# Performance work log

Hardware: AMD Instinct MI355X
Metric: run time of the kernel (lower is better)

Reference implementation:

```python
import jax, jax.numpy as jnp
import numpy as np

N_NODES = 10000
N_EDGES = 160000
N_HEADS = 2
N_IN = 16   # fc input dim = x channels (15) + 1 dist channel
N_OUT = 32
ALPHA = 0.2
B, T_LEN = 2, 8


def setup_inputs() -> dict:
    key = jax.random.key(0)
    ks = jax.random.split(key, 6)
    x = jax.random.normal(ks[0], (B, T_LEN, N_NODES, N_IN - 1), dtype=jnp.float32)
    d_ew = jax.random.uniform(ks[1], (N_EDGES + N_NODES, N_HEADS), dtype=jnp.float32)
    u_edges = jax.random.randint(ks[2], (N_EDGES, 2), 0, N_NODES, dtype=jnp.int64)
    u_dist = jax.random.uniform(ks[3], (N_EDGES,), dtype=jnp.float32)
    W = jax.random.normal(ks[4], (N_OUT, N_IN), dtype=jnp.float32) * (1.0 / np.sqrt(N_IN))
    b = jax.random.normal(ks[5], (N_OUT,), dtype=jnp.float32) * 0.01
    return {"x": x, "T": T_LEN, "d_ew": d_ew, "u_edges": u_edges,
            "u_dist": u_dist, "W": W, "b": b}


def reference(x, T, d_ew, u_edges, u_dist, W, b):
    # d_edges = [u_edges; self-loops], d_dist = [u_dist; zeros]
    loops = jnp.arange(N_NODES, dtype=u_edges.dtype)
    d_edges = jnp.concatenate([u_edges, jnp.stack([loops, loops], axis=1)], axis=0)
    d_dist = jnp.concatenate([u_dist, jnp.zeros((N_NODES,), dtype=u_dist.dtype)], axis=0)
    node_i, node_j = d_edges[:, 0], d_edges[:, 1]

    Bx, t, _, C = x.shape
    # graph convolution: out[:, :, j] = sum_e{j(e)=j} d_ew[e] * x[:, :, i(e)]
    xg = x[:, :, node_i, :]                               # (B, t, E, C)
    msgs = xg[..., None, :] * d_ew[None, None, :, :, None]  # (B, t, E, H, C)
    x_conv = jnp.zeros((Bx, t, N_NODES, N_HEADS, C), dtype=x.dtype)
    x_conv = x_conv.at[:, :, node_j].add(msgs)            # (B, t, N, H, C)

    # dist convolution: (N, H)
    dist_conv = jnp.zeros((N_NODES, N_HEADS), dtype=d_ew.dtype)
    dist_conv = dist_conv.at[node_j].add(d_dist[:, None] * d_ew)

    # concat dist channel, broadcast over (B, t)
    dist_b = jnp.broadcast_to(dist_conv[None, None, :, :, None],
                              (Bx, t, N_NODES, N_HEADS, 1))
    x_feature = jnp.concatenate([x_conv, dist_b], axis=-1)  # (B, t, N, H, C+1)

    x_out = jnp.einsum('btnhc,oc->btnho', x_feature, W) + b

    # temporal alpha-blend (RHS uses pre-update values, as in torch slice assign)
    x_out = jnp.concatenate(
        [x_out[:, :1], ALPHA * x_out[:, :-1] + (1.0 - ALPHA) * x_out[:, 1:]], axis=1)
    return jax.nn.sigmoid(x_out)
```

## Files before the change

### kernel.cpp

```cpp
#include <hip/hip_runtime.h>
#include <hip/hip_bf16.h>

#define NN 10000
#define NE 160000
#define NBT 16
#define CIN 15
#define HPAD 128
#define BCAP 64
#define NOUT 32
#define ALPHA_F 0.2f

#define TRANS_BLKS 625
#define EDGE_BLKS  625

__device__ __forceinline__ float bf2f(unsigned short u) {
    return __uint_as_float(((unsigned int)u) << 16);
}
__device__ __forceinline__ unsigned short f2bf(float f) {
    __hip_bfloat16 h = __float2bfloat16(f);
    return *(unsigned short*)&h;
}

__global__ __launch_bounds__(256) void zero_ws(int* __restrict__ p) {
    int i = blockIdx.x * 256 + threadIdx.x;
    if (i < NN) p[i] = 0;
}

__global__ __launch_bounds__(256) void prep(const float* __restrict__ x,
                                            const int* __restrict__ edges,
                                            const float* __restrict__ dist,
                                            const float* __restrict__ dew,
                                            unsigned short* __restrict__ xh,
                                            int* __restrict__ cursor,
                                            int2* __restrict__ epay) {
    __shared__ float tile[NBT][16 * CIN];
    int bid = blockIdx.x;
    int tid = threadIdx.x;
    if (bid < TRANS_BLKS) {
        int n0 = bid * 16;
        if (tid < 16 * CIN) {
#pragma unroll
            for (int bt = 0; bt < NBT; ++bt)
                tile[bt][tid] = x[((size_t)bt * NN + n0) * CIN + tid];
        }
        __syncthreads();
        for (int g = tid; g < 16 * 256; g += 256) {
            int ln = g >> 8;
            int r  = g & 255;
            int c  = r & 15;
            int bt = r >> 4;
            float v = (c < 15) ? tile[bt][ln * CIN + c] : 0.f;
            xh[(size_t)(n0 + ln) * 256 + r] = f2bf(v);
        }
    } else {
        int e = (bid - TRANS_BLKS) * 256 + tid;
        if (e < NE) {
            int2 ed = ((const int2*)edges)[e];
            float2 w = ((const float2*)dew)[e];
            float d = dist[e];
            int pos = atomicAdd(&cursor[ed.y], 1);
            if (pos < BCAP) {
                unsigned int px = (unsigned int)ed.x | ((unsigned int)f2bf(d) << 16);
                unsigned int py = (unsigned int)f2bf(w.x) | ((unsigned int)f2bf(w.y) << 16);
                epay[ed.y * BCAP + pos] = make_int2((int)px, (int)py);
            }
        }
    }
}

__global__ __launch_bounds__(256) void fused_node(const unsigned short* __restrict__ xh,
                                                  const int* __restrict__ cursor,
                                                  const int2* __restrict__ epay,
                                                  const float* __restrict__ dew,
                                                  const float* __restrict__ W,
                                                  const float* __restrict__ bias,
                                                  float* __restrict__ out) {
    __shared__ float s_xc[4][2][256];

    const int tid = threadIdx.x;
    const int unit = tid >> 6;
    const int lane = tid & 63;
    const int n = blockIdx.x * 4 + unit;
    const int o = lane & 31;
    const int h = lane >> 5;

    float4 w0_ = *(const float4*)(W + o * 16);
    float4 w1_ = *(const float4*)(W + o * 16 + 4);
    float4 w2_ = *(const float4*)(W + o * 16 + 8);
    float4 w3_ = *(const float4*)(W + o * 16 + 12);
    float bo = bias[o];

    int deg = cursor[n];
    if (deg > BCAP) deg = BCAP;

    int2 pay = epay[n * BCAP + lane];

    float dd  = bf2f((unsigned short)((unsigned int)pay.x >> 16));
    float w0l = bf2f((unsigned short)((unsigned int)pay.y & 0xFFFFu));
    float w1l = bf2f((unsigned short)((unsigned int)pay.y >> 16));
    float dc0 = (lane < deg) ? dd * w0l : 0.f;
    float dc1 = (lane < deg) ? dd * w1l : 0.f;
#pragma unroll
    for (int m = 32; m; m >>= 1) {
        dc0 += __shfl_xor(dc0, m, 64);
        dc1 += __shfl_xor(dc1, m, 64);
    }

    const char* xbase = (const char*)xh + 8 * lane;
    float a00 = 0.f, a01 = 0.f, a02 = 0.f, a03 = 0.f;
    float a10 = 0.f, a11 = 0.f, a12 = 0.f, a13 = 0.f;
#pragma unroll 8
    for (int k = 0; k < deg; ++k) {
        int sx = __builtin_amdgcn_readlane(pay.x, k);
        int sw = __builtin_amdgcn_readlane(pay.y, k);
        uint2 u = *(const uint2*)(xbase + (size_t)((sx & 0xFFFF) << 9));
        float x0 = __uint_as_float(u.x << 16);
        float x1 = __uint_as_float(u.x & 0xFFFF0000u);
        float x2 = __uint_as_float(u.y << 16);
        float x3 = __uint_as_float(u.y & 0xFFFF0000u);
        float w0 = __uint_as_float((unsigned int)sw << 16);
        float w1 = __uint_as_float((unsigned int)sw & 0xFFFF0000u);
        a00 += w0 * x0; a01 += w0 * x1; a02 += w0 * x2; a03 += w0 * x3;
        a10 += w1 * x0; a11 += w1 * x1; a12 += w1 * x2; a13 += w1 * x3;
    }
    {
        uint2 u = *(const uint2*)(xbase + ((size_t)n << 9));
        float w0 = dew[2 * (NE + n) + 0];
        float w1 = dew[2 * (NE + n) + 1];
        float x0 = __uint_as_float(u.x << 16);
        float x1 = __uint_as_float(u.x & 0xFFFF0000u);
        float x2 = __uint_as_float(u.y << 16);
        float x3 = __uint_as_float(u.y & 0xFFFF0000u);
        a00 += w0 * x0; a01 += w0 * x1; a02 += w0 * x2; a03 += w0 * x3;
        a10 += w1 * x0; a11 += w1 * x1; a12 += w1 * x2; a13 += w1 * x3;
    }
    *(float4*)&s_xc[unit][0][4 * lane] = make_float4(a00, a01, a02, a03);
    *(float4*)&s_xc[unit][1][4 * lane] = make_float4(a10, a11, a12, a13);

    asm volatile("s_waitcnt lgkmcnt(0)" ::: "memory");

    {
        float Wr[16] = { w0_.x, w0_.y, w0_.z, w0_.w,
                         w1_.x, w1_.y, w1_.z, w1_.w,
                         w2_.x, w2_.y, w2_.z, w2_.w,
                         w3_.x, w3_.y, w3_.z, w3_.w };
        float base = bo + Wr[15] * (h ? dc1 : dc0);
        const float* xc = s_xc[unit][h];
#pragma unroll
        for (int b = 0; b < 2; ++b) {
            float prev = 0.f;
#pragma unroll
            for (int t = 0; t < 8; ++t) {
                const float* xt = xc + b * HPAD + t * 16;
                float4 v0 = *(const float4*)(xt);
                float4 v1 = *(const float4*)(xt + 4);
                float4 v2 = *(const float4*)(xt + 8);
                float4 v3 = *(const float4*)(xt + 12);
                float y = base;
                y += Wr[0]*v0.x + Wr[1]*v0.y + Wr[2]*v0.z + Wr[3]*v0.w;
                y += Wr[4]*v1.x + Wr[5]*v1.y + Wr[6]*v1.z + Wr[7]*v1.w;
                y += Wr[8]*v2.x + Wr[9]*v2.y + Wr[10]*v2.z + Wr[11]*v2.w;
                y += Wr[12]*v3.x + Wr[13]*v3.y + Wr[14]*v3.z + Wr[15]*v3.w;
                float v = (t == 0) ? y : (ALPHA_F * prev + (1.f - ALPHA_F) * y);
                float sg = 1.f / (1.f + __expf(-v));
                __builtin_nontemporal_store(sg,
                    &out[(((size_t)(b * 8 + t) * NN + n) * 2 + h) * NOUT + o]);
                prev = y;
            }
        }
    }
}

extern "C" void kernel_launch(void* const* d_in, const int* in_sizes, int n_in,
                              void* d_out, int out_size, void* d_ws, size_t ws_size,
                              hipStream_t stream) {
    const float* x     = (const float*)d_in[0];
    const float* dew   = (const float*)d_in[2];
    const int*   edges = (const int*)d_in[3];
    const float* dist  = (const float*)d_in[4];
    const float* W     = (const float*)d_in[5];
    const float* bias  = (const float*)d_in[6];
    float* out = (float*)d_out;

    unsigned short* xh = (unsigned short*)d_ws;
    int2* epay   = (int2*)(xh + (size_t)NN * 256);
    int* cursor  = (int*)(epay + (size_t)NN * BCAP);

    zero_ws<<<(NN + 255) / 256, 256, 0, stream>>>(cursor);
    prep<<<TRANS_BLKS + EDGE_BLKS, 256, 0, stream>>>(x, edges, dist, dew,
                                                     xh, cursor, epay);
    fused_node<<<2500, 256, 0, stream>>>(xh, cursor, epay, dew, W, bias, out);
}
```

Baseline: 49.99 us.

## Process two nodes per wavefront in fused node kernel to increase gather ILP

Each 64-lane wavefront now handles two destination nodes, with each half-wave loading one node's edge payload. The gather loop interleaves two independent edge streams, so more loads are in flight per iteration. Grid size is halved accordingly. In exchange it uses more registers, pays for the max of the two degrees, and adds an overflow path for degree above 32.

```diff
diff --git a/kernel.cpp b/kernel.cpp
--- a/kernel.cpp
+++ b/kernel.cpp
@@ -75,14 +75,16 @@
                                                   const float* __restrict__ W,
                                                   const float* __restrict__ bias,
                                                   float* __restrict__ out) {
-    __shared__ float s_xc[4][2][256];
-
-    const int tid = threadIdx.x;
+    __shared__ float s_xc[4][2][2][256];
+
+    const int tid  = threadIdx.x;
     const int unit = tid >> 6;
     const int lane = tid & 63;
-    const int n = blockIdx.x * 4 + unit;
-    const int o = lane & 31;
-    const int h = lane >> 5;
+    const int sub  = lane & 31;
+    const int h    = lane >> 5;
+    const int o    = lane & 31;
+    const int nA   = blockIdx.x * 8 + unit * 2;
+    const int nB   = nA + 1;
 
     float4 w0_ = *(const float4*)(W + o * 16);
     float4 w1_ = *(const float4*)(W + o * 16 + 4);
@@ -90,82 +92,171 @@
     float4 w3_ = *(const float4*)(W + o * 16 + 12);
     float bo = bias[o];
 
-    int deg = cursor[n];
-    if (deg > BCAP) deg = BCAP;
-
-    int2 pay = epay[n * BCAP + lane];
-
-    float dd  = bf2f((unsigned short)((unsigned int)pay.x >> 16));
-    float w0l = bf2f((unsigned short)((unsigned int)pay.y & 0xFFFFu));
-    float w1l = bf2f((unsigned short)((unsigned int)pay.y >> 16));
-    float dc0 = (lane < deg) ? dd * w0l : 0.f;
-    float dc1 = (lane < deg) ? dd * w1l : 0.f;
-#pragma unroll
-    for (int m = 32; m; m >>= 1) {
-        dc0 += __shfl_xor(dc0, m, 64);
-        dc1 += __shfl_xor(dc1, m, 64);
+    int degA = cursor[nA]; degA = degA > BCAP ? BCAP : degA;
+    int degB = cursor[nB]; degB = degB > BCAP ? BCAP : degB;
+    const int myN   = h ? nB : nA;
+    const int myDeg = h ? degB : degA;
+
+    int2 pay  = epay[myN * BCAP + sub];
+    int2 pay2 = make_int2(0, 0);
+    if (degA > 32 || degB > 32)
+        pay2 = epay[myN * BCAP + 32 + sub];
+
+    float dc0, dc1;
+    {
+        float dd  = bf2f((unsigned short)((unsigned int)pay.x >> 16));
+        float w0l = bf2f((unsigned short)((unsigned int)pay.y & 0xFFFFu));
+        float w1l = bf2f((unsigned short)((unsigned int)pay.y >> 16));
+        dc0 = (sub < myDeg) ? dd * w0l : 0.f;
+        dc1 = (sub < myDeg) ? dd * w1l : 0.f;
+        float dd2 = bf2f((unsigned short)((unsigned int)pay2.x >> 16));
+        float w02 = bf2f((unsigned short)((unsigned int)pay2.y & 0xFFFFu));
+        float w12 = bf2f((unsigned short)((unsigned int)pay2.y >> 16));
+        if (sub + 32 < myDeg) { dc0 += dd2 * w02; dc1 += dd2 * w12; }
+#pragma unroll
+        for (int m = 16; m; m >>= 1) {
+            dc0 += __shfl_xor(dc0, m, 64);
+            dc1 += __shfl_xor(dc1, m, 64);
+        }
     }
 
     const char* xbase = (const char*)xh + 8 * lane;
-    float a00 = 0.f, a01 = 0.f, a02 = 0.f, a03 = 0.f;
-    float a10 = 0.f, a11 = 0.f, a12 = 0.f, a13 = 0.f;
-#pragma unroll 8
-    for (int k = 0; k < deg; ++k) {
-        int sx = __builtin_amdgcn_readlane(pay.x, k);
-        int sw = __builtin_amdgcn_readlane(pay.y, k);
-        uint2 u = *(const uint2*)(xbase + (size_t)((sx & 0xFFFF) << 9));
+    float aA0=0,aA1=0,aA2=0,aA3=0,aA4=0,aA5=0,aA6=0,aA7=0;
+    float aB0=0,aB1=0,aB2=0,aB3=0,aB4=0,aB5=0,aB6=0,aB7=0;
+
+    int dmax  = degA > degB ? degA : degB;
+    int dmain = dmax > 32 ? 32 : dmax;
+#pragma unroll 4
+    for (int k = 0; k < dmain; ++k) {
+        {
+            int kk = (k < degA) ? k : 0;
+            unsigned int px = (unsigned int)__builtin_amdgcn_readlane(pay.x, kk);
+            unsigned int pw = (unsigned int)__builtin_amdgcn_readlane(pay.y, kk);
+            unsigned int src = px & 0xFFFFu; src = src < NN ? src : 0;
+            uint2 u = *(const uint2*)(xbase + (src << 9));
+            float vw0 = (k < degA) ? __uint_as_float(pw << 16) : 0.f;
+            float vw1 = (k < degA) ? __uint_as_float(pw & 0xFFFF0000u) : 0.f;
+            float x0 = __uint_as_float(u.x << 16);
+            float x1 = __uint_as_float(u.x & 0xFFFF0000u);
+            float x2 = __uint_as_float(u.y << 16);
+            float x3 = __uint_as_float(u.y & 0xFFFF0000u);
+            aA0 += vw0*x0; aA1 += vw0*x1; aA2 += vw0*x2; aA3 += vw0*x3;
+            aA4 += vw1*x0; aA5 += vw1*x1; aA6 += vw1*x2; aA7 += vw1*x3;
+        }
+        {
+            int kk = (k < degB) ? k : 0;
+            unsigned int px = (unsigned int)__builtin_amdgcn_readlane(pay.x, 32 + kk);
+            unsigned int pw = (unsigned int)__builtin_amdgcn_readlane(pay.y, 32 + kk);
+            unsigned int src = px & 0xFFFFu; src = src < NN ? src : 0;
+            uint2 u = *(const uint2*)(xbase + (src << 9));
+            float vw0 = (k < degB) ? __uint_as_float(pw << 16) : 0.f;
+            float vw1 = (k < degB) ? __uint_as_float(pw & 0xFFFF0000u) : 0.f;
+            float x0 = __uint_as_float(u.x << 16);
+            float x1 = __uint_as_float(u.x & 0xFFFF0000u);
+            float x2 = __uint_as_float(u.y << 16);
+            float x3 = __uint_as_float(u.y & 0xFFFF0000u);
+            aB0 += vw0*x0; aB1 += vw0*x1; aB2 += vw0*x2; aB3 += vw0*x3;
+            aB4 += vw1*x0; aB5 += vw1*x1; aB6 += vw1*x2; aB7 += vw1*x3;
+        }
+    }
+    if (dmax > 32) {
+        for (int k = 32; k < dmax; ++k) {
+            {
+                int kk = (k < degA) ? k - 32 : 0;
+                unsigned int px = (unsigned int)__builtin_amdgcn_readlane(pay2.x, kk);
+                unsigned int pw = (unsigned int)__builtin_amdgcn_readlane(pay2.y, kk);
+                unsigned int src = px & 0xFFFFu; src = src < NN ? src : 0;
+                uint2 u = *(const uint2*)(xbase + (src << 9));
+                float vw0 = (k < degA) ? __uint_as_float(pw << 16) : 0.f;
+                float vw1 = (k < degA) ? __uint_as_float(pw & 0xFFFF0000u) : 0.f;
+                float x0 = __uint_as_float(u.x << 16);
+                float x1 = __uint_as_float(u.x & 0xFFFF0000u);
+                float x2 = __uint_as_float(u.y << 16);
+                float x3 = __uint_as_float(u.y & 0xFFFF0000u);
+                aA0 += vw0*x0; aA1 += vw0*x1; aA2 += vw0*x2; aA3 += vw0*x3;
+                aA4 += vw1*x0; aA5 += vw1*x1; aA6 += vw1*x2; aA7 += vw1*x3;
+            }
+            {
+                int kk = (k < degB) ? k - 32 : 0;
+                unsigned int px = (unsigned int)__builtin_amdgcn_readlane(pay2.x, 32 + kk);
+                unsigned int pw = (unsigned int)__builtin_amdgcn_readlane(pay2.y, 32 + kk);
+                unsigned int src = px & 0xFFFFu; src = src < NN ? src : 0;
+                uint2 u = *(const uint2*)(xbase + (src << 9));
+                float vw0 = (k < degB) ? __uint_as_float(pw << 16) : 0.f;
+                float vw1 = (k < degB) ? __uint_as_float(pw & 0xFFFF0000u) : 0.f;
+                float x0 = __uint_as_float(u.x << 16);
+                float x1 = __uint_as_float(u.x & 0xFFFF0000u);
+                float x2 = __uint_as_float(u.y << 16);
+                float x3 = __uint_as_float(u.y & 0xFFFF0000u);
+                aB0 += vw0*x0; aB1 += vw0*x1; aB2 += vw0*x2; aB3 += vw0*x3;
+                aB4 += vw1*x0; aB5 += vw1*x1; aB6 += vw1*x2; aB7 += vw1*x3;
+            }
+        }
+    }
+    {
+        uint2 u = *(const uint2*)(xbase + ((size_t)nA << 9));
+        float sw0 = dew[2 * (NE + nA) + 0];
+        float sw1 = dew[2 * (NE + nA) + 1];
         float x0 = __uint_as_float(u.x << 16);
         float x1 = __uint_as_float(u.x & 0xFFFF0000u);
         float x2 = __uint_as_float(u.y << 16);
         float x3 = __uint_as_float(u.y & 0xFFFF0000u);
-        float w0 = __uint_as_float((unsigned int)sw << 16);
-        float w1 = __uint_as_float((unsigned int)sw & 0xFFFF0000u);
-        a00 += w0 * x0; a01 += w0 * x1; a02 += w0 * x2; a03 += w0 * x3;
-        a10 += w1 * x0; a11 += w1 * x1; a12 += w1 * x2; a13 += w1 * x3;
-    }
-    {
-        uint2 u = *(const uint2*)(xbase + ((size_t)n << 9));
-        float w0 = dew[2 * (NE + n) + 0];
-        float w1 = dew[2 * (NE + n) + 1];
-        float x0 = __uint_as_float(u.x << 16);
-        float x1 = __uint_as_float(u.x & 0xFFFF0000u);
-        float x2 = __uint_as_float(u.y << 16);
-        float x3 = __uint_as_float(u.y & 0xFFFF0000u);
-        a00 += w0 * x0; a01 += w0 * x1; a02 += w0 * x2; a03 += w0 * x3;
-        a10 += w1 * x0; a11 += w1 * x1; a12 += w1 * x2; a13 += w1 * x3;
-    }
-    *(float4*)&s_xc[unit][0][4 * lane] = make_float4(a00, a01, a02, a03);
-    *(float4*)&s_xc[unit][1][4 * lane] = make_float4(a10, a11, a12, a13);
+        aA0 += sw0*x0; aA1 += sw0*x1; aA2 += sw0*x2; aA3 += sw0*x3;
+        aA4 += sw1*x0; aA5 += sw1*x1; aA6 += sw1*x2; aA7 += sw1*x3;
+        uint2 v = *(const uint2*)(xbase + ((size_t)nB << 9));
+        float tw0 = dew[2 * (NE + nB) + 0];
+        float tw1 = dew[2 * (NE + nB) + 1];
+        float y0 = __uint_as_float(v.x << 16);
+        float y1 = __uint_as_float(v.x & 0xFFFF0000u);
+        float y2 = __uint_as_float(v.y << 16);
+        float y3 = __uint_as_float(v.y & 0xFFFF0000u);
+        aB0 += tw0*y0; aB1 += tw0*y1; aB2 += tw0*y2; aB3 += tw0*y3;
+        aB4 += tw1*y0; aB5 += tw1*y1; aB6 += tw1*y2; aB7 += tw1*y3;
+    }
+
+    *(float4*)&s_xc[unit][0][0][4 * lane] = make_float4(aA0, aA1, aA2, aA3);
+    *(float4*)&s_xc[unit][0][1][4 * lane] = make_float4(aA4, aA5, aA6, aA7);
+    *(float4*)&s_xc[unit][1][0][4 * lane] = make_float4(aB0, aB1, aB2, aB3);
+    *(float4*)&s_xc[unit][1][1][4 * lane] = make_float4(aB4, aB5, aB6, aB7);
 
     asm volatile("s_waitcnt lgkmcnt(0)" ::: "memory");
+
+    float dcA0 = __shfl(dc0, 0, 64),  dcA1 = __shfl(dc1, 0, 64);
+    float dcB0 = __shfl(dc0, 32, 64), dcB1 = __shfl(dc1, 32, 64);
+    float dcA = h ? dcA1 : dcA0;
+    float dcB = h ? dcB1 : dcB0;
 
     {
         float Wr[16] = { w0_.x, w0_.y, w0_.z, w0_.w,
                          w1_.x, w1_.y, w1_.z, w1_.w,
                          w2_.x, w2_.y, w2_.z, w2_.w,
                          w3_.x, w3_.y, w3_.z, w3_.w };
-        float base = bo + Wr[15] * (h ? dc1 : dc0);
-        const float* xc = s_xc[unit][h];
-#pragma unroll
-        for (int b = 0; b < 2; ++b) {
-            float prev = 0.f;
-#pragma unroll
-            for (int t = 0; t < 8; ++t) {
-                const float* xt = xc + b * HPAD + t * 16;
-                float4 v0 = *(const float4*)(xt);
-                float4 v1 = *(const float4*)(xt + 4);
-                float4 v2 = *(const float4*)(xt + 8);
-                float4 v3 = *(const float4*)(xt + 12);
-                float y = base;
-                y += Wr[0]*v0.x + Wr[1]*v0.y + Wr[2]*v0.z + Wr[3]*v0.w;
-                y += Wr[4]*v1.x + Wr[5]*v1.y + Wr[6]*v1.z + Wr[7]*v1.w;
-                y += Wr[8]*v2.x + Wr[9]*v2.y + Wr[10]*v2.z + Wr[11]*v2.w;
-                y += Wr[12]*v3.x + Wr[13]*v3.y + Wr[14]*v3.z + Wr[15]*v3.w;
-                float v = (t == 0) ? y : (ALPHA_F * prev + (1.f - ALPHA_F) * y);
-                float sg = 1.f / (1.f + __expf(-v));
-                __builtin_nontemporal_store(sg,
-                    &out[(((size_t)(b * 8 + t) * NN + n) * 2 + h) * NOUT + o]);
-                prev = y;
+#pragma unroll
+        for (int nd = 0; nd < 2; ++nd) {
+            float base = bo + Wr[15] * (nd ? dcB : dcA);
+            const float* xc = s_xc[unit][nd][h];
+            const int n = nA + nd;
+#pragma unroll
+            for (int b = 0; b < 2; ++b) {
+                float prev = 0.f;
+#pragma unroll
+                for (int t = 0; t < 8; ++t) {
+                    const float* xt = xc + b * HPAD + t * 16;
+                    float4 v0 = *(const float4*)(xt);
+                    float4 v1 = *(const float4*)(xt + 4);
+                    float4 v2 = *(const float4*)(xt + 8);
+                    float4 v3 = *(const float4*)(xt + 12);
+                    float y = base;
+                    y += Wr[0]*v0.x + Wr[1]*v0.y + Wr[2]*v0.z + Wr[3]*v0.w;
+                    y += Wr[4]*v1.x + Wr[5]*v1.y + Wr[6]*v1.z + Wr[7]*v1.w;
+                    y += Wr[8]*v2.x + Wr[9]*v2.y + Wr[10]*v2.z + Wr[11]*v2.w;
+                    y += Wr[12]*v3.x + Wr[13]*v3.y + Wr[14]*v3.z + Wr[15]*v3.w;
+                    float v = (t == 0) ? y : (ALPHA_F * prev + (1.f - ALPHA_F) * y);
+                    float sg = 1.f / (1.f + __expf(-v));
+                    __builtin_nontemporal_store(sg,
+                        &out[(((size_t)(b * 8 + t) * NN + n) * 2 + h) * NOUT + o]);
+                    prev = y;
+                }
             }
         }
     }
@@ -189,5 +280,5 @@
     zero_ws<<<(NN + 255) / 256, 256, 0, stream>>>(cursor);
     prep<<<TRANS_BLKS + EDGE_BLKS, 256, 0, stream>>>(x, edges, dist, dew,
                                                      xh, cursor, epay);
-    fused_node<<<2500, 256, 0, stream>>>(xh, cursor, epay, dew, W, bias, out);
-}
+    fused_node<<<1250, 256, 0, stream>>>(xh, cursor, epay, dew, W, bias, out);
+}
```

After: 50.53 us. Within noise of the previous version (+1.1%).

## Process two nodes per wave with wider 16-byte gathers over edge pairs

Applied to the files above, without the earlier changes.

Each wavefront now handles two destination nodes, and each half-wave takes alternate edges with 16-byte bf16 loads covering 8 channels per lane. The halves are combined by a cross-half shuffle. The distance term is folded into the padded channel slot of the gather instead of a separate wave reduction. This aims to halve the serial edge-loop trip count and use wider loads to hide gather latency. In exchange it adds extra shuffles, more registers and a second payload load for degrees above 32, and the grid is halved.

```diff
diff --git a/kernel.cpp b/kernel.cpp
--- a/kernel.cpp
+++ b/kernel.cpp
@@ -20,6 +20,8 @@
     __hip_bfloat16 h = __float2bfloat16(f);
     return *(unsigned short*)&h;
 }
+__device__ __forceinline__ float bfl(unsigned int u) { return __uint_as_float(u << 16); }
+__device__ __forceinline__ float bfh(unsigned int u) { return __uint_as_float(u & 0xFFFF0000u); }
 
 __global__ __launch_bounds__(256) void zero_ws(int* __restrict__ p) {
     int i = blockIdx.x * 256 + threadIdx.x;
@@ -68,6 +70,108 @@
     }
 }
 
+__device__ __forceinline__ void gather_node(
+    int n, int deg, int2 pay, const int2* __restrict__ bucket,
+    const char* __restrict__ xh_b, const float* __restrict__ dew,
+    int lane, bool ispad, float* __restrict__ sdst ) {
+    const int sub = lane & 31;
+    const int half = lane >> 5;
+    const char* xlane = xh_b + 16 * sub;
+    float ac0[8] = {0,0,0,0,0,0,0,0};
+    float ac1[8] = {0,0,0,0,0,0,0,0};
+
+    int dmain = deg > 32 ? 32 : deg;
+    int pairs = (dmain + 1) >> 1;
+#pragma unroll 4
+    for (int i = 0; i < pairs; ++i) {
+        int sx = __shfl(pay.x, 2 * i, 32);
+        int sw = __shfl(pay.y, 2 * i, 32);
+        bool val = (2 * i + half) < deg;
+        unsigned int su = (unsigned int)sx & 0x3FFFu;
+        uint4 u = *(const uint4*)(xlane + ((size_t)su << 9));
+        float w0 = val ? bfh((unsigned int)sw << 16) : 0.f;
+        float w1 = val ? bfh((unsigned int)sw) : 0.f;
+        float de = bfh((unsigned int)sx);
+        float x0 = bfl(u.x), x1 = bfh(u.x), x2 = bfl(u.y), x3 = bfh(u.y);
+        float x4 = bfl(u.z), x5 = bfh(u.z), x6 = bfl(u.w);
+        float x7 = ispad ? de : bfh(u.w);
+        ac0[0]+=w0*x0; ac0[1]+=w0*x1; ac0[2]+=w0*x2; ac0[3]+=w0*x3;
+        ac0[4]+=w0*x4; ac0[5]+=w0*x5; ac0[6]+=w0*x6; ac0[7]+=w0*x7;
+        ac1[0]+=w1*x0; ac1[1]+=w1*x1; ac1[2]+=w1*x2; ac1[3]+=w1*x3;
+        ac1[4]+=w1*x4; ac1[5]+=w1*x5; ac1[6]+=w1*x6; ac1[7]+=w1*x7;
+    }
+    if (deg > 32) {
+        int2 payB = bucket[32 + sub + half];
+        int pairsB = (deg - 32 + 1) >> 1;
+        for (int i = 0; i < pairsB; ++i) {
+            int sx = __shfl(payB.x, 2 * i, 32);
+            int sw = __shfl(payB.y, 2 * i, 32);
+            bool val = (32 + 2 * i + half) < deg;
+            unsigned int su = (unsigned int)sx & 0x3FFFu;
+            uint4 u = *(const uint4*)(xlane + ((size_t)su << 9));
+            float w0 = val ? bfh((unsigned int)sw << 16) : 0.f;
+            float w1 = val ? bfh((unsigned int)sw) : 0.f;
+            float de = bfh((unsigned int)sx);
+            float x0 = bfl(u.x), x1 = bfh(u.x), x2 = bfl(u.y), x3 = bfh(u.y);
+            float x4 = bfl(u.z), x5 = bfh(u.z), x6 = bfl(u.w);
+            float x7 = ispad ? de : bfh(u.w);
+            ac0[0]+=w0*x0; ac0[1]+=w0*x1; ac0[2]+=w0*x2; ac0[3]+=w0*x3;
+            ac0[4]+=w0*x4; ac0[5]+=w0*x5; ac0[6]+=w0*x6; ac0[7]+=w0*x7;
+            ac1[0]+=w1*x0; ac1[1]+=w1*x1; ac1[2]+=w1*x2; ac1[3]+=w1*x3;
+            ac1[4]+=w1*x4; ac1[5]+=w1*x5; ac1[6]+=w1*x6; ac1[7]+=w1*x7;
+        }
+    }
+#pragma unroll
+    for (int j = 0; j < 8; ++j) {
+        ac0[j] += __shfl_xor(ac0[j], 32, 64);
+        ac1[j] += __shfl_xor(ac1[j], 32, 64);
+    }
+    {
+        uint4 u = *(const uint4*)(xlane + ((size_t)n << 9));
+        float w0 = dew[2 * (NE + n) + 0];
+        float w1 = dew[2 * (NE + n) + 1];
+        float xs[8] = { bfl(u.x), bfh(u.x), bfl(u.y), bfh(u.y),
+                        bfl(u.z), bfh(u.z), bfl(u.w), bfh(u.w) };
+#pragma unroll
+        for (int j = 0; j < 8; ++j) { ac0[j] += w0 * xs[j]; ac1[j] += w1 * xs[j]; }
+    }
+    float v0 = half ? ac1[0] : ac0[0], v1 = half ? ac1[1] : ac0[1];
+    float v2 = half ? ac1[2] : ac0[2], v3 = half ? ac1[3] : ac0[3];
+    float v4 = half ? ac1[4] : ac0[4], v5 = half ? ac1[5] : ac0[5];
+    float v6 = half ? ac1[6] : ac0[6], v7 = half ? ac1[7] : ac0[7];
+    float* dst = sdst + half * 256 + 8 * sub;
+    *(float4*)(dst)     = make_float4(v0, v1, v2, v3);
+    *(float4*)(dst + 4) = make_float4(v4, v5, v6, v7);
+}
+
+__device__ __forceinline__ void finalize_node(
+    int n, const float* __restrict__ sdst, const float* __restrict__ Wr,
+    float bo, int h, int o, float* __restrict__ out) {
+    const float* xc = sdst + h * 256;
+#pragma unroll
+    for (int b = 0; b < 2; ++b) {
+        float prev = 0.f;
+#pragma unroll
+        for (int t = 0; t < 8; ++t) {
+            const float* xt = xc + b * HPAD + t * 16;
+            float4 v0 = *(const float4*)(xt);
+            float4 v1 = *(const float4*)(xt + 4);
+            float4 v2 = *(const float4*)(xt + 8);
+            float4 v3 = *(const float4*)(xt + 12);
+            float y = bo;
+            y += Wr[0]*v0.x + Wr[1]*v0.y + Wr[2]*v0.z + Wr[3]*v0.w;
+            y += Wr[4]*v1.x + Wr[5]*v1.y + Wr[6]*v1.z + Wr[7]*v1.w;
+            y += Wr[8]*v2.x + Wr[9]*v2.y + Wr[10]*v2.z + Wr[11]*v2.w;
+            y += Wr[12]*v3.x + Wr[13]*v3.y + Wr[14]*v3.z + Wr[15]*v3.w;
+            float v = (t == 0) ? y : (ALPHA_F * prev + (1.f - ALPHA_F) * y);
+            float sg = 1.f / (1.f + __expf(-v));
+            __builtin_nontemporal_store(sg,
+                &out[(((size_t)(b * 8 + t) * NN + n) * 2 + h) * NOUT + o]);
+            prev = y;
+        }
+    }
+}
+
 __global__ __launch_bounds__(256) void fused_node(const unsigned short* __restrict__ xh,
                                                   const int* __restrict__ cursor,
                                                   const int2* __restrict__ epay,
@@ -75,100 +179,42 @@
                                                   const float* __restrict__ W,
                                                   const float* __restrict__ bias,
                                                   float* __restrict__ out) {
-    __shared__ float s_xc[4][2][256];
+    __shared__ float s_xc[4][2][2][256];
 
     const int tid = threadIdx.x;
     const int unit = tid >> 6;
     const int lane = tid & 63;
-    const int n = blockIdx.x * 4 + unit;
     const int o = lane & 31;
     const int h = lane >> 5;
+    const bool ispad = (lane & 1);
+    const int wid = blockIdx.x * 4 + unit;
+    const int n1 = wid * 2;
+    const int n2 = n1 + 1;
+
+    int deg1 = cursor[n1]; if (deg1 > BCAP) deg1 = BCAP;
+    int deg2 = cursor[n2]; if (deg2 > BCAP) deg2 = BCAP;
+    const int idx = (lane & 31) + (lane >> 5);
+    int2 pay1 = epay[n1 * BCAP + idx];
+    int2 pay2 = epay[n2 * BCAP + idx];
 
     float4 w0_ = *(const float4*)(W + o * 16);
     float4 w1_ = *(const float4*)(W + o * 16 + 4);
     float4 w2_ = *(const float4*)(W + o * 16 + 8);
     float4 w3_ = *(const float4*)(W + o * 16 + 12);
     float bo = bias[o];
-
-    int deg = cursor[n];
-    if (deg > BCAP) deg = BCAP;
-
-    int2 pay = epay[n * BCAP + lane];
-
-    float dd  = bf2f((unsigned short)((unsigned int)pay.x >> 16));
-    float w0l = bf2f((unsigned short)((unsigned int)pay.y & 0xFFFFu));
-    float w1l = bf2f((unsigned short)((unsigned int)pay.y >> 16));
-    float dc0 = (lane < deg) ? dd * w0l : 0.f;
-    float dc1 = (lane < deg) ? dd * w1l : 0.f;
-#pragma unroll
-    for (int m = 32; m; m >>= 1) {
-        dc0 += __shfl_xor(dc0, m, 64);
-        dc1 += __shfl_xor(dc1, m, 64);
-    }
-
-    const char* xbase = (const char*)xh + 8 * lane;
-    float a00 = 0.f, a01 = 0.f, a02 = 0.f, a03 = 0.f;
-    float a10 = 0.f, a11 = 0.f, a12 = 0.f, a13 = 0.f;
-#pragma unroll 8
-    for (int k = 0; k < deg; ++k) {
-        int sx = __builtin_amdgcn_readlane(pay.x, k);
-        int sw = __builtin_amdgcn_readlane(pay.y, k);
-        uint2 u = *(const uint2*)(xbase + (size_t)((sx & 0xFFFF) << 9));
-        float x0 = __uint_as_float(u.x << 16);
-        float x1 = __uint_as_float(u.x & 0xFFFF0000u);
-        float x2 = __uint_as_float(u.y << 16);
-        float x3 = __uint_as_float(u.y & 0xFFFF0000u);
-        float w0 = __uint_as_float((unsigned int)sw << 16);
-        float w1 = __uint_as_float((unsigned int)sw & 0xFFFF0000u);
-        a00 += w0 * x0; a01 += w0 * x1; a02 += w0 * x2; a03 += w0 * x3;
-        a10 += w1 * x0; a11 += w1 * x1; a12 += w1 * x2; a13 += w1 * x3;
-    }
-    {
-        uint2 u = *(const uint2*)(xbase + ((size_t)n << 9));
-        float w0 = dew[2 * (NE + n) + 0];
-        float w1 = dew[2 * (NE + n) + 1];
-        float x0 = __uint_as_float(u.x << 16);
-        float x1 = __uint_as_float(u.x & 0xFFFF0000u);
-        float x2 = __uint_as_float(u.y << 16);
-        float x3 = __uint_as_float(u.y & 0xFFFF0000u);
-        a00 += w0 * x0; a01 += w0 * x1; a02 += w0 * x2; a03 += w0 * x3;
-        a10 += w1 * x0; a11 += w1 * x1; a12 += w1 * x2; a13 += w1 * x3;
-    }
-    *(float4*)&s_xc[unit][0][4 * lane] = make_float4(a00, a01, a02, a03);
-    *(float4*)&s_xc[unit][1][4 * lane] = make_float4(a10, a11, a12, a13);
+    float Wr[16] = { w0_.x, w0_.y, w0_.z, w0_.w,  w1_.x, w1_.y, w1_.z, w1_.w,
+                     w2_.x, w2_.y, w2_.z, w2_.w,  w3_.x, w3_.y, w3_.z, w3_.w };
+
+    const char* xh_b = (const char*)xh;
+    gather_node(n1, deg1, pay1, epay + n1 * BCAP, xh_b, dew, lane, ispad,
+                &s_xc[unit][0][0][0]);
+    gather_node(n2, deg2, pay2, epay + n2 * BCAP, xh_b, dew, lane, ispad,
+                &s_xc[unit][1][0][0]);
 
     asm volatile("s_waitcnt lgkmcnt(0)" ::: "memory");
 
-    {
-        float Wr[16] = { w0_.x, w0_.y, w0_.z, w0_.w,
-                         w1_.x, w1_.y, w1_.z, w1_.w,
-                         w2_.x, w2_.y, w2_.z, w2_.w,
-                         w3_.x, w3_.y, w3_.z, w3_.w };
-        float base = bo + Wr[15] * (h ? dc1 : dc0);
-        const float* xc = s_xc[unit][h];
-#pragma unroll
-        for (int b = 0; b < 2; ++b) {
-            float prev = 0.f;
-#pragma unroll
-            for (int t = 0; t < 8; ++t) {
-                const float* xt = xc + b * HPAD + t * 16;
-                float4 v0 = *(const float4*)(xt);
-                float4 v1 = *(const float4*)(xt + 4);
-                float4 v2 = *(const float4*)(xt + 8);
-                float4 v3 = *(const float4*)(xt + 12);
-                float y = base;
-                y += Wr[0]*v0.x + Wr[1]*v0.y + Wr[2]*v0.z + Wr[3]*v0.w;
-                y += Wr[4]*v1.x + Wr[5]*v1.y + Wr[6]*v1.z + Wr[7]*v1.w;
-                y += Wr[8]*v2.x + Wr[9]*v2.y + Wr[10]*v2.z + Wr[11]*v2.w;
-                y += Wr[12]*v3.x + Wr[13]*v3.y + Wr[14]*v3.z + Wr[15]*v3.w;
-                float v = (t == 0) ? y : (ALPHA_F * prev + (1.f - ALPHA_F) * y);
-                float sg = 1.f / (1.f + __expf(-v));
-                __builtin_nontemporal_store(sg,
-                    &out[(((size_t)(b * 8 + t) * NN + n) * 2 + h) * NOUT + o]);
-                prev = y;
-            }
-        }
-    }
+    finalize_node(n1, &s_xc[unit][0][0][0], Wr, bo, h, o, out);
+    finalize_node(n2, &s_xc[unit][1][0][0], Wr, bo, h, o, out);
 }
 
 extern "C" void kernel_launch(void* const* d_in, const int* in_sizes, int n_in,
@@ -189,5 +235,5 @@
     zero_ws<<<(NN + 255) / 256, 256, 0, stream>>>(cursor);
     prep<<<TRANS_BLKS + EDGE_BLKS, 256, 0, stream>>>(x, edges, dist, dew,
                                                      xh, cursor, epay);
-    fused_node<<<2500, 256, 0, stream>>>(xh, cursor, epay, dew, W, bias, out);
-}
+    fused_node<<<1250, 256, 0, stream>>>(xh, cursor, epay, dew, W, bias, out);
+}
```

Result: faster. 48.66 us (-2.6%).
